# Performance work log

Measured on AMD Instinct MI355X. Metric: run time of the kernel, lower is better.

The kernel has to match this reference:

```python
import jax, jax.numpy as jnp
import numpy as np

DIM, HEADS, DH, P, C = 2048, 8, 256, 7, 128
NP = (56 // P) ** 2          # 64 patches
N = NP + 1 + NP              # 65 pos tokens concatenated with 64 patch tokens = 129
PATCH_FEAT = C * P * P       # 6272
LN_EPS = 1e-5


def patchify(x, p):
    # 'b c (h p1) (w p2) -> b (h w) (p1 p2 c)'
    b, c, H, W = x.shape
    h, w = H // p, W // p
    x = x.reshape(b, c, h, p, w, p).transpose(0, 2, 4, 3, 5, 1)
    return x.reshape(b, h * w, p * p * c)


def setup_inputs() -> dict:
    key = jax.random.key(0)
    ks = jax.random.split(key, 16)
    s = 0.02
    d = dict(
        x_q=jax.random.normal(ks[0], (64, C, 56, 56), jnp.float32),
        x_kv=jax.random.normal(ks[1], (64, C, 56, 56), jnp.float32),
        W_ex=jax.random.normal(ks[2], (PATCH_FEAT, DIM), jnp.float32) * s,
        b_ex=jnp.zeros((DIM,), jnp.float32),
        W_en=jax.random.normal(ks[3], (PATCH_FEAT, DIM), jnp.float32) * s,
        b_en=jnp.zeros((DIM,), jnp.float32),
        pos=jax.random.normal(ks[4], (1, NP + 1, DIM), jnp.float32),
        Wq=jax.random.normal(ks[5], (DIM, HEADS * DH), jnp.float32) * s,
        Wk=jax.random.normal(ks[6], (DIM, HEADS * DH), jnp.float32) * s,
        Wv=jax.random.normal(ks[7], (DIM, HEADS * DH), jnp.float32) * s,
        Wo=jax.random.normal(ks[8], (HEADS * DH, DIM), jnp.float32) * s,
        bo=jnp.zeros((DIM,), jnp.float32),
        gamma=jnp.ones((DIM,), jnp.float32),
        beta=jnp.zeros((DIM,), jnp.float32),
        Wh=jax.random.normal(ks[9], (DIM, PATCH_FEAT), jnp.float32) * s,
        bh=jnp.zeros((PATCH_FEAT,), jnp.float32),
        Wm=jax.random.normal(ks[10], (DH, N), jnp.float32) * s,
        bm=jnp.zeros((N,), jnp.float32),
    )
    return d


def reference(x_q, x_kv, W_ex, b_ex, W_en, b_en, pos, Wq, Wk, Wv, Wo, bo,
              gamma, beta, Wh, bh, Wm, bm):
    b = x_q.shape[0]
    scale = DH ** -0.5
    # image embedder: patch embed + concat pos tokens
    tq = patchify(x_q, P) @ W_ex + b_ex                      # [b, 64, DIM]
    tk = patchify(x_kv, P) @ W_en + b_en                     # [b, 64, DIM]
    posb = jnp.broadcast_to(pos, (b, NP + 1, DIM))
    tq = jnp.concatenate([posb, tq], axis=1)                 # [b, N, DIM]
    tk = jnp.concatenate([posb, tk], axis=1)                 # [b, N, DIM]

    def split_heads(t):
        return t.reshape(b, N, HEADS, DH).transpose(0, 2, 1, 3)  # b h n d

    q = split_heads(tq @ Wq)
    k = split_heads(tk @ Wk)
    v = split_heads(tk @ Wv)

    # VAE-style reparameterize: mu=k, logvar=q
    eps = jax.random.normal(jax.random.key(42), k.shape, k.dtype)
    z = k + jnp.exp(0.5 * q) * eps                           # [b, h, n, d]

    # scale + linear remap d -> N, softmax, weighted sum with v
    dots = (z * scale) @ Wm + bm                             # [b, h, n, N]
    attn = jax.nn.softmax(dots, axis=-1)
    out = jnp.einsum('bhij,bhjd->bhid', attn, v)             # [b, h, n, d]
    out = out.transpose(0, 2, 1, 3).reshape(b, N, HEADS * DH)
    out = out @ Wo + bo                                      # [b, N, DIM]

    # mlp head: LayerNorm + Linear (final rearrange-to-image is shape-only, omitted)
    mu = out.mean(-1, keepdims=True)
    var = ((out - mu) ** 2).mean(-1, keepdims=True)
    ln = (out - mu) * jax.lax.rsqrt(var + LN_EPS) * gamma + beta
    head = ln @ Wh + bh                                      # [b, N, 6272]

    qf = q.reshape(b, -1)
    kf = k.reshape(b, -1)
    qn = qf / jnp.linalg.norm(qf, axis=1, keepdims=True)
    kn = kf / jnp.linalg.norm(kf, axis=1, keepdims=True)
    return head, qn, kn
```

## Files before the change

kernel.cpp:

```cpp
#include <hip/hip_runtime.h>


typedef unsigned short u16;
typedef short bf16x8 __attribute__((ext_vector_type(8)));
typedef unsigned short u16x8 __attribute__((ext_vector_type(8)));
typedef float f32x4 __attribute__((ext_vector_type(4)));

#define WAITV(N) asm volatile("s_waitcnt vmcnt(" #N ")" ::: "memory")

static __device__ __forceinline__ void barx() {
    asm volatile("" ::: "memory");
    __builtin_amdgcn_s_barrier();
    asm volatile("" ::: "memory");
}

static __device__ __forceinline__ u16 f2b(float f) {
    union { float f; unsigned int u; } cv; cv.f = f;
    unsigned int u = cv.u;
    unsigned int lsb = (u >> 16) & 1u;
    u += 0x7fffu + lsb;
    return (u16)(u >> 16);
}

static __device__ __forceinline__ float b2f(u16 u) {
    union { unsigned int i; float f; } c; c.i = ((unsigned int)u) << 16; return c.f;
}

static __device__ __forceinline__ void gemm8p_body(
    const u16* __restrict__ A, const u16* __restrict__ Bt, void* __restrict__ Cv,
    const float* __restrict__ bias, int M, int N, int K,
    int lda, int ldb, int ldc, float alpha, int c_bf16, int row_remap,
    int m0, int n0, u16* lds)
{
    const int tid = threadIdx.x, lane = tid & 63, wave = tid >> 6;
    const int wm = wave >> 2, wn = wave & 3;
    const int l15 = lane & 15, l4 = lane >> 4;
    const int scol = (((lane & 3) ^ ((lane >> 3) & 3)) << 3);
    const int bswz = ((l4 ^ ((l15 >> 1) & 3)) << 3);

    f32x4 acc[8][4] = {};
    const int nt = K >> 6;
    const int niter = nt >> 1;

    auto STAGE = [&](int tt, int kh, int isB) {
        const int c = tt & 1;
        const int k0 = (tt << 6) + (kh << 5);
        const int rbase = isB ? n0 : m0;
        const u16* P = isB ? Bt : A;
        const int ld = isB ? ldb : lda;
        const int lim = isB ? N : M;
        const int dbase = c * 32768 + isB * 16384 + kh * 8192;
        #pragma unroll
        for (int j = 0; j < 2; ++j) {
            const int r0 = j * 128 + wave * 16;
            int g = rbase + r0 + (lane >> 2); g = g < lim ? g : lim - 1;
            const u16* src = P + (long)g * ld + k0 + scol;
            __builtin_amdgcn_global_load_lds(
                (const __attribute__((address_space(1))) void*)src,
                (__attribute__((address_space(3))) void*)&lds[dbase + r0 * 32],
                16, 0, 0);
        }
    };

    bf16x8 bfr[4];
    auto LOADB = [&](int c, int kk) {
        #pragma unroll
        for (int nn = 0; nn < 4; ++nn) {
            const int row = wn * 64 + nn * 16 + l15;
            bfr[nn] = *(const bf16x8*)&lds[c * 32768 + 16384 + kk * 8192 + row * 32 + bswz];
        }
    };
    auto LDA = [&](int c, int kk, int mh, bf16x8* af) {
        #pragma unroll
        for (int mm = 0; mm < 4; ++mm) {
            const int row = wm * 128 + mh * 64 + mm * 16 + l15;
            af[mm] = *(const bf16x8*)&lds[c * 32768 + kk * 8192 + row * 32 + bswz];
        }
    };
    auto MM = [&](const bf16x8* af, int mh) {
        __builtin_amdgcn_s_setprio(1);
        #pragma unroll
        for (int mm = 0; mm < 4; ++mm)
            #pragma unroll
            for (int nn = 0; nn < 4; ++nn)
                acc[mh * 4 + mm][nn] = __builtin_amdgcn_mfma_f32_16x16x32_bf16(
                    af[mm], bfr[nn], acc[mh * 4 + mm][nn], 0, 0, 0);
        __builtin_amdgcn_s_setprio(0);
    };

    STAGE(0, 0, 0); STAGE(0, 0, 1); STAGE(0, 1, 0); STAGE(0, 1, 1);
    STAGE(1, 0, 0); STAGE(1, 0, 1);

    bf16x8 a0[4], a1[4];
    for (int i = 0; i < niter; ++i) {
        const int t0 = 2 * i, t1 = t0 + 1;
        const bool has2 = (t0 + 2 < nt);
        WAITV(8); barx();
        LOADB(0, 0); LDA(0, 0, 0, a0);
        STAGE(t1, 1, 0); STAGE(t1, 1, 1);
        MM(a0, 0); LDA(0, 0, 1, a1); MM(a1, 1);
        WAITV(8); barx();
        LOADB(0, 1); LDA(0, 1, 0, a0);
        if (has2) { STAGE(t0 + 2, 0, 0); STAGE(t0 + 2, 0, 1); }
        MM(a0, 0); LDA(0, 1, 1, a1); MM(a1, 1);
        if (has2) { WAITV(8); } else { WAITV(4); }
        barx();
        LOADB(1, 0); LDA(1, 0, 0, a0);
        if (has2) { STAGE(t0 + 2, 1, 0); STAGE(t0 + 2, 1, 1); }
        MM(a0, 0); LDA(1, 0, 1, a1); MM(a1, 1);
        if (has2) { WAITV(8); } else { WAITV(0); }
        barx();
        LOADB(1, 1); LDA(1, 1, 0, a0);
        if (has2) { STAGE(t1 + 2, 0, 0); STAGE(t1 + 2, 0, 1); }
        MM(a0, 0); LDA(1, 1, 1, a1); MM(a1, 1);
    }

    #pragma unroll
    for (int mr = 0; mr < 8; ++mr) {
        #pragma unroll
        for (int nn = 0; nn < 4; ++nn) {
            const int col = n0 + wn * 64 + nn * 16 + l15;
            if (col >= N) continue;
            const float bv = bias ? bias[col] : 0.0f;
            #pragma unroll
            for (int jj = 0; jj < 4; ++jj) {
                const int row = m0 + wm * 128 + mr * 16 + l4 * 4 + jj;
                if (row >= M) continue;
                float v = alpha * acc[mr][nn][jj] + bv;
                long crow = row;
                if (row_remap) crow = (long)(row >> 6) * 129 + 65 + (row & 63);
                if (c_bf16) ((u16*)Cv)[crow * (long)ldc + col] = f2b(v);
                else        ((float*)Cv)[crow * (long)ldc + col] = v;
            }
        }
    }
}

__global__ __launch_bounds__(512, 2) void gemm_8p(
    const u16* __restrict__ A, const u16* __restrict__ Bt, void* __restrict__ Cv,
    const float* __restrict__ bias, int M, int N, int K,
    int lda, int ldb, int ldc, float alpha, int c_bf16, int row_remap)
{
    __shared__ u16 lds[65536];
    gemm8p_body(A, Bt, Cv, bias, M, N, K, lda, ldb, ldc, alpha, c_bf16, row_remap,
                blockIdx.x * 256, blockIdx.y * 256, lds);
}

__global__ __launch_bounds__(512, 2) void gemm_8p3(
    const u16* A0, const u16* A1, const u16* A2,
    const u16* B0, const u16* B1, const u16* B2,
    u16* C0, u16* C1, u16* C2,
    const float* bias0, const float* bias1, const float* bias2,
    int M, int N, int K, int lda, int ldb, int ldc, float alpha, int row_remap)
{
    __shared__ u16 lds[65536];
    const int z = blockIdx.z;
    const u16* A = z == 0 ? A0 : (z == 1 ? A1 : A2);
    const u16* B = z == 0 ? B0 : (z == 1 ? B1 : B2);
    u16* C = z == 0 ? C0 : (z == 1 ? C1 : C2);
    const float* bias = z == 0 ? bias0 : (z == 1 ? bias1 : bias2);
    gemm8p_body(A, B, C, bias, M, N, K, lda, ldb, ldc, alpha, 1, row_remap,
                blockIdx.x * 256, blockIdx.y * 256, lds);
}

__global__ __launch_bounds__(256, 2) void gemm_pipe(
    const u16* __restrict__ A, const u16* __restrict__ Bt, void* __restrict__ Cv,
    const float* __restrict__ bias, int M, int N, int K,
    int lda, int ldb, int ldc, float alpha, int c_bf16)
{
    __shared__ u16 lds[2 * 16384];

    const int tid = threadIdx.x, lane = tid & 63, wave = tid >> 6;
    const int wm = wave >> 1, wn = wave & 1;
    const int l15 = lane & 15, l4 = lane >> 4;

    const int srow = tid >> 3;
    const int scol = (((tid & 7) * 16) ^ (((tid >> 3) & 7) << 4)) >> 1;
    const int cf0 = (((0 * 64) + l4 * 16) ^ ((l15 & 7) << 4)) >> 1;
    const int cf1 = (((1 * 64) + l4 * 16) ^ ((l15 & 7) << 4)) >> 1;

    const int nt = K >> 6;
    const int nbx = (M + 127) >> 7, nby = N >> 7;
    const int ntiles = nbx * nby;

    for (int tile = blockIdx.x; tile < ntiles; tile += gridDim.x) {
        const int m0 = (tile / nby) * 128, n0 = (tile % nby) * 128;

        auto STAGE = [&](int c, int t) {
            const int k0 = t << 6;
            #pragma unroll
            for (int j = 0; j < 4; ++j) {
                const int r = j * 32 + srow;
                int ga = m0 + r; ga = ga < M ? ga : M - 1;
                const u16* srcA = A + (long)ga * lda + k0 + scol;
                __builtin_amdgcn_global_load_lds(
                    (const __attribute__((address_space(1))) void*)srcA,
                    (__attribute__((address_space(3))) void*)&lds[c * 16384 + j * 2048 + wave * 512],
                    16, 0, 0);
                int gb = n0 + r; gb = gb < N ? gb : N - 1;
                const u16* srcB = Bt + (long)gb * ldb + k0 + scol;
                __builtin_amdgcn_global_load_lds(
                    (const __attribute__((address_space(1))) void*)srcB,
                    (__attribute__((address_space(3))) void*)&lds[c * 16384 + 8192 + j * 2048 + wave * 512],
                    16, 0, 0);
            }
        };

        f32x4 acc[4][4] = {};
        STAGE(0, 0);
        __syncthreads();
        for (int t = 0; t < nt; ++t) {
            const int c = t & 1;
            if (t + 1 < nt) STAGE(c ^ 1, t + 1);
            const int ab = c * 16384, bb = ab + 8192;
            #pragma unroll
            for (int kk = 0; kk < 2; ++kk) {
                const int cf = kk ? cf1 : cf0;
                bf16x8 af[4], bfr[4];
                #pragma unroll
                for (int m = 0; m < 4; ++m)
                    af[m] = *(const bf16x8*)&lds[ab + (wm * 64 + m * 16 + l15) * 64 + cf];
                #pragma unroll
                for (int n = 0; n < 4; ++n)
                    bfr[n] = *(const bf16x8*)&lds[bb + (wn * 64 + n * 16 + l15) * 64 + cf];
                __builtin_amdgcn_s_setprio(1);
                #pragma unroll
                for (int m = 0; m < 4; ++m)
                    #pragma unroll
                    for (int n = 0; n < 4; ++n)
                        acc[m][n] = __builtin_amdgcn_mfma_f32_16x16x32_bf16(
                            af[m], bfr[n], acc[m][n], 0, 0, 0);
                __builtin_amdgcn_s_setprio(0);
            }
            __syncthreads();
        }

        #pragma unroll
        for (int m = 0; m < 4; ++m) {
            #pragma unroll
            for (int n = 0; n < 4; ++n) {
                const int col = n0 + wn * 64 + n * 16 + l15;
                if (col >= N) continue;
                const float bv = bias ? bias[col] : 0.0f;
                #pragma unroll
                for (int j = 0; j < 4; ++j) {
                    const int row = m0 + wm * 64 + m * 16 + l4 * 4 + j;
                    if (row >= M) continue;
                    float v = alpha * acc[m][n][j] + bv;
                    if (c_bf16) ((u16*)Cv)[(long)row * ldc + col] = f2b(v);
                    else        ((float*)Cv)[(long)row * ldc + col] = v;
                }
            }
        }
    }
}

__global__ __launch_bounds__(256) void gemm_bt(
    const u16* __restrict__ A, const u16* __restrict__ Bt, void* __restrict__ Cv,
    const float* __restrict__ bias, int M, int N, int K,
    int lda, int ldb, int ldc, float alpha, int c_bf16, int row_remap,
    long sA, long sB, long sCo, long sCi, int binner)
{
    const int bz = blockIdx.z;
    const u16* Ab = A + (long)bz * sA;
    const u16* Bb = Bt + (long)bz * sB;
    const long cOff = (long)(bz / binner) * sCo + (long)(bz % binner) * sCi;

    __shared__ u16 As[128][72];
    __shared__ u16 Bs[128][72];

    const int tid = threadIdx.x;
    const int lane = tid & 63;
    const int wave = tid >> 6;
    const int wr = wave >> 1, wc = wave & 1;
    const int l15 = lane & 15, l4 = lane >> 4;
    const int m0 = blockIdx.x * 128, n0 = blockIdx.y * 128;

    const int r = tid >> 3;
    const int kof = (tid & 7) * 8;

    f32x4 acc[4][4] = {};

    const int ktiles = (K + 63) / 64;
    for (int kt = 0; kt < ktiles; ++kt) {
        const int k0 = kt * 64;
        __syncthreads();
        #pragma unroll
        for (int i = 0; i < 4; ++i) {
            const int row = r + 32 * i;
            const int gk = k0 + kof;
            u16x8 v = {0,0,0,0,0,0,0,0};
            const int grow = m0 + row;
            if (grow < M && gk < K)
                v = *(const u16x8*)(Ab + (long)grow * lda + gk);
            *(u16x8*)&As[row][kof] = v;
        }
        #pragma unroll
        for (int i = 0; i < 4; ++i) {
            const int row = r + 32 * i;
            const int gk = k0 + kof;
            u16x8 v = {0,0,0,0,0,0,0,0};
            const int gcol = n0 + row;
            if (gcol < N && gk < K)
                v = *(const u16x8*)(Bb + (long)gcol * ldb + gk);
            *(u16x8*)&Bs[row][kof] = v;
        }
        __syncthreads();
        #pragma unroll
        for (int ks = 0; ks < 2; ++ks) {
            bf16x8 af[4], bfr[4];
            #pragma unroll
            for (int m = 0; m < 4; ++m)
                af[m] = *(const bf16x8*)&As[wr*64 + m*16 + l15][ks*32 + l4*8];
            #pragma unroll
            for (int n = 0; n < 4; ++n)
                bfr[n] = *(const bf16x8*)&Bs[wc*64 + n*16 + l15][ks*32 + l4*8];
            #pragma unroll
            for (int m = 0; m < 4; ++m)
                #pragma unroll
                for (int n = 0; n < 4; ++n)
                    acc[m][n] = __builtin_amdgcn_mfma_f32_16x16x32_bf16(
                        af[m], bfr[n], acc[m][n], 0, 0, 0);
        }
    }

    #pragma unroll
    for (int m = 0; m < 4; ++m) {
        #pragma unroll
        for (int n = 0; n < 4; ++n) {
            const int col = n0 + wc*64 + n*16 + l15;
            if (col >= N) continue;
            const float bv = bias ? bias[col] : 0.0f;
            #pragma unroll
            for (int j = 0; j < 4; ++j) {
                const int row = m0 + wr*64 + m*16 + l4*4 + j;
                if (row >= M) continue;
                float v = alpha * acc[m][n][j] + bv;
                long crow = row;
                if (row_remap) crow = (long)(row >> 6) * 129 + 65 + (row & 63);
                if (c_bf16) ((u16*)Cv)[cOff + crow * (long)ldc + col] = f2b(v);
                else        ((float*)Cv)[cOff + crow * (long)ldc + col] = v;
            }
        }
    }
}

__global__ __launch_bounds__(256, 2) void fdots_kernel(
    const u16* __restrict__ z, const u16* __restrict__ Wm_t,
    const float* __restrict__ bm, u16* __restrict__ attn)
{
    __shared__ u16 wlds[144 * 264];
    const int tid = threadIdx.x;
    for (int i = tid; i < 144 * 32; i += 256) {
        const int row = i >> 5, c8 = i & 31;
        *(u16x8*)&wlds[row * 264 + c8 * 8] = *(const u16x8*)&Wm_t[row * 256 + c8 * 8];
    }
    __syncthreads();
    const int lane = tid & 63, wave = tid >> 6;
    const int l15 = lane & 15, l4 = lane >> 4;

    float bmv[9];
    #pragma unroll
    for (int c = 0; c < 9; ++c) {
        const int col = c * 16 + l15;
        bmv[c] = (col < 129) ? bm[col] : 0.0f;
    }

    for (int rg = blockIdx.x; rg < 516; rg += gridDim.x) {
        const long rowbase = (long)rg * 128 + wave * 32;

        f32x4 acc[2][9] = {};
        #pragma unroll
        for (int kk = 0; kk < 8; ++kk) {
            bf16x8 af[2];
            #pragma unroll
            for (int rgp = 0; rgp < 2; ++rgp)
                af[rgp] = *(const bf16x8*)&z[(rowbase + rgp * 16 + l15) * 256 + kk * 32 + l4 * 8];
            #pragma unroll
            for (int c = 0; c < 9; ++c) {
                const bf16x8 bf = *(const bf16x8*)&wlds[(c * 16 + l15) * 264 + kk * 32 + l4 * 8];
                #pragma unroll
                for (int rgp = 0; rgp < 2; ++rgp)
                    acc[rgp][c] = __builtin_amdgcn_mfma_f32_16x16x32_bf16(af[rgp], bf, acc[rgp][c], 0, 0, 0);
            }
        }

        #pragma unroll
        for (int rgp = 0; rgp < 2; ++rgp) {
            #pragma unroll
            for (int j = 0; j < 4; ++j) {
                float v[9]; float mx = -1e30f;
                #pragma unroll
                for (int c = 0; c < 9; ++c) {
                    const int col = c * 16 + l15;
                    v[c] = (col < 129) ? (0.0625f * acc[rgp][c][j] + bmv[c]) : -1e30f;
                    mx = fmaxf(mx, v[c]);
                }
                #pragma unroll
                for (int o = 1; o < 16; o <<= 1) mx = fmaxf(mx, __shfl_xor(mx, o, 64));
                float s = 0.f;
                #pragma unroll
                for (int c = 0; c < 9; ++c) {
                    v[c] = (c * 16 + l15 < 129) ? expf(v[c] - mx) : 0.0f;
                    s += v[c];
                }
                #pragma unroll
                for (int o = 1; o < 16; o <<= 1) s += __shfl_xor(s, o, 64);
                const float inv = 1.0f / s;
                u16* ar = attn + (rowbase + rgp * 16 + l4 * 4 + j) * 144;
                #pragma unroll
                for (int c = 0; c < 9; ++c)
                    ar[c * 16 + l15] = f2b(v[c] * inv);
            }
        }
    }
}

__global__ __launch_bounds__(256) void row128_kernel(
    const u16* __restrict__ attn, const u16* __restrict__ v_t, u16* __restrict__ outm)
{
    const int bh = blockIdx.x, d = threadIdx.x;
    const int b = bh >> 3, h = bh & 7;
    __shared__ float a[144];
    for (int j = threadIdx.x; j < 144; j += 256)
        a[j] = (j < 129) ? b2f(attn[((long)bh * 129 + 128) * 144 + j]) : 0.0f;
    __syncthreads();
    const u16* vr = v_t + ((long)bh * 256 + d) * 144;
    float s = 0.f;
    #pragma unroll
    for (int j8 = 0; j8 < 18; ++j8) {
        const bf16x8 vv = *(const bf16x8*)&vr[j8 * 8];
        #pragma unroll
        for (int e = 0; e < 8; ++e) s += a[j8 * 8 + e] * b2f((u16)vv[e]);
    }
    outm[((long)(b * 129 + 128)) * 2048 + h * 256 + d] = f2b(s);
}

__global__ __launch_bounds__(256) void transpose_conv4(
    const float* in0, const float* in1, const float* in2, const float* in3,
    u16* o0, u16* o1, u16* o2, u16* o3, int K, int N, int KP, int NPd)
{
    const int zz = blockIdx.z;
    const float* in = zz == 0 ? in0 : (zz == 1 ? in1 : (zz == 2 ? in2 : in3));
    u16* out = zz == 0 ? o0 : (zz == 1 ? o1 : (zz == 2 ? o2 : o3));
    __shared__ float tile[32][33];
    const int k0 = blockIdx.x * 32, n0 = blockIdx.y * 32;
    const int tx = threadIdx.x, ty = threadIdx.y;
    #pragma unroll
    for (int i = 0; i < 4; ++i) {
        const int k = k0 + ty + i*8, n = n0 + tx;
        tile[ty + i*8][tx] = (k < K && n < N) ? in[(long)k * N + n] : 0.0f;
    }
    __syncthreads();
    #pragma unroll
    for (int i = 0; i < 4; ++i) {
        const int n = n0 + ty + i*8, k = k0 + tx;
        if (n < NPd && k < KP) out[(long)n * KP + k] = f2b(tile[tx][ty + i*8]);
    }
}

__global__ __launch_bounds__(256) void patchify_kernel(
    const float* __restrict__ xq, const float* __restrict__ xkv,
    u16* __restrict__ oq, u16* __restrict__ okv)
{
    __shared__ u16 tile[64 * 7 * 58];
    const int zz = blockIdx.z;
    const float* x = (zz >= 64) ? xkv : xq;
    u16* out = (zz >= 64) ? okv : oq;
    const int b = zz & 63, hh = blockIdx.y, cg = blockIdx.x;
    const int c0 = cg * 64;
    for (int i = threadIdx.x; i < 64 * 392; i += 256) {
        const int c = i / 392, rem = i - c * 392;
        const int p1 = rem / 56, w = rem - p1 * 56;
        const float v = x[(((long)b * 128 + c0 + c) * 56 + hh * 7 + p1) * 56 + w];
        tile[(c * 7 + p1) * 58 + w] = f2b(v);
    }
    __syncthreads();
    #pragma unroll
    for (int ww = 0; ww < 8; ++ww) {
        const long base = ((long)(b * 64 + hh * 8 + ww)) * 6272 + c0;
        for (int j = threadIdx.x; j < 49 * 64; j += 256) {
            const int c = j & 63, pp = j >> 6;
            const int p1 = pp / 7, p2 = pp - p1 * 7;
            out[base + pp * 128 + c] = tile[(c * 7 + p1) * 58 + ww * 7 + p2];
        }
    }
}

__global__ __launch_bounds__(256) void posfill_kernel(
    const float* __restrict__ pos, u16* __restrict__ Tq, u16* __restrict__ Tk)
{
    const int t = blockIdx.x, b = blockIdx.y;
    const int c0 = threadIdx.x * 8;
    const float* pr = pos + (long)t * 2048 + c0;
    u16x8 v;
    #pragma unroll
    for (int e = 0; e < 8; ++e) v[e] = f2b(pr[e]);
    const long idx = ((long)b * 129 + t) * 2048 + c0;
    *(u16x8*)&Tq[idx] = v;
    *(u16x8*)&Tk[idx] = v;
}

__global__ void vtrans_kernel(const u16* __restrict__ vmat, u16* __restrict__ v_t)
{
    const int bh = blockIdx.z; const int b = bh >> 3, h = bh & 7;
    const int d0 = blockIdx.x * 32, n0 = blockIdx.y * 32;
    __shared__ u16 tile[32][33];
    const int tx = threadIdx.x, ty = threadIdx.y;
    #pragma unroll
    for (int i = 0; i < 4; ++i) {
        const int n = n0 + ty + i*8;
        if (n < 129)
            tile[ty + i*8][tx] = vmat[((long)b*129 + n) * 2048 + h*256 + d0 + tx];
    }
    __syncthreads();
    #pragma unroll
    for (int i = 0; i < 4; ++i) {
        const int d = d0 + ty + i*8, n = n0 + tx;
        if (n < 144)
            v_t[((long)bh * 256 + d) * 144 + n] = (n < 129) ? tile[tx][ty + i*8] : (u16)0;
    }
}

static __device__ __forceinline__ unsigned int rotl32(unsigned int x, int d) {
    return (x << d) | (x >> (32 - d));
}

static __device__ __forceinline__ float threefry_normal(unsigned int i) {
    const unsigned int ks0 = 0u, ks1 = 42u;
    const unsigned int ks2 = ks0 ^ ks1 ^ 0x1BD11BDAu;
    unsigned int x0 = 0u + ks0;
    unsigned int x1 = i + ks1;
#define TF_R(rr) { x0 += x1; x1 = rotl32(x1, rr); x1 ^= x0; }
    TF_R(13) TF_R(15) TF_R(26) TF_R(6)
    x0 += ks1; x1 += ks2 + 1u;
    TF_R(17) TF_R(29) TF_R(16) TF_R(24)
    x0 += ks2; x1 += ks0 + 2u;
    TF_R(13) TF_R(15) TF_R(26) TF_R(6)
    x0 += ks0; x1 += ks1 + 3u;
    TF_R(17) TF_R(29) TF_R(16) TF_R(24)
    x0 += ks1; x1 += ks2 + 4u;
    TF_R(13) TF_R(15) TF_R(26) TF_R(6)
    x0 += ks2; x1 += ks0 + 5u;
#undef TF_R
    const unsigned int bits = x0 ^ x1;
    const unsigned int fb = (bits >> 9) | 0x3f800000u;
    union { unsigned int u; float f; } cv; cv.u = fb;
    const float f = cv.f - 1.0f;
    const float lo = -0.99999994f;
    float u = f * (1.0f - lo) + lo;
    u = fmaxf(lo, u);
    return 1.4142135623730951f * erfinvf(u);
}

__global__ __launch_bounds__(256) void z_kernel(
    const u16* __restrict__ qmat, const u16* __restrict__ kmat,
    const float* __restrict__ norms, u16* __restrict__ z,
    float* __restrict__ outq, float* __restrict__ outk)
{
    const unsigned int i = blockIdx.x * 256u + threadIdx.x;
    const int d = i & 255; const unsigned int t = i >> 8;
    const int n = t % 129; const int bh = t / 129;
    const int b = bh >> 3, h = bh & 7;
    const long src = ((long)(b * 129 + n)) * 2048 + h * 256 + d;
    const float qf = b2f(qmat[src]);
    const float kf = b2f(kmat[src]);
    const float eps = threefry_normal(i);
    z[i] = f2b(kf + expf(0.5f * qf) * eps);
    outq[i] = qf / norms[b];
    outk[i] = kf / norms[64 + b];
}

__global__ __launch_bounds__(256) void ln_kernel(
    const float* __restrict__ proj, const float* __restrict__ gamma,
    const float* __restrict__ beta, u16* __restrict__ ln)
{
    const int row = blockIdx.x;
    const float* p = proj + (long)row * 2048;
    const int tid = threadIdx.x;
    float v[8]; float s = 0.f, s2 = 0.f;
    #pragma unroll
    for (int i = 0; i < 8; ++i) {
        v[i] = p[tid + i * 256]; s += v[i]; s2 += v[i] * v[i];
    }
    #pragma unroll
    for (int o = 32; o > 0; o >>= 1) { s += __shfl_down(s, o, 64); s2 += __shfl_down(s2, o, 64); }
    __shared__ float sh[8];
    if ((tid & 63) == 0) { sh[tid >> 6] = s; sh[4 + (tid >> 6)] = s2; }
    __syncthreads();
    s = sh[0] + sh[1] + sh[2] + sh[3];
    s2 = sh[4] + sh[5] + sh[6] + sh[7];
    const float mu = s * (1.0f / 2048.0f);
    const float var = s2 * (1.0f / 2048.0f) - mu * mu;
    const float rinv = 1.0f / sqrtf(var + 1e-5f);
    u16* lr = ln + (long)row * 2048;
    #pragma unroll
    for (int i = 0; i < 8; ++i) {
        const int c = tid + i * 256;
        lr[c] = f2b((v[i] - mu) * rinv * gamma[c] + beta[c]);
    }
}

__global__ __launch_bounds__(256) void norm_reduce(
    const u16* __restrict__ qmat, const u16* __restrict__ kmat, float* __restrict__ norms)
{
    const int b = blockIdx.x & 63;
    const u16* src = (blockIdx.x >= 64 ? kmat : qmat) + (long)b * 264192;
    float s = 0.f;
    for (int i = threadIdx.x; i < 264192; i += 256) { const float x = b2f(src[i]); s += x * x; }
    #pragma unroll
    for (int o = 32; o > 0; o >>= 1) s += __shfl_down(s, o, 64);
    __shared__ float sh[4];
    if ((threadIdx.x & 63) == 0) sh[threadIdx.x >> 6] = s;
    __syncthreads();
    if (threadIdx.x == 0) norms[blockIdx.x] = sqrtf(sh[0] + sh[1] + sh[2] + sh[3]);
}

extern "C" void kernel_launch(void* const* d_in, const int* in_sizes, int n_in,
                              void* d_out, int out_size, void* d_ws, size_t ws_size,
                              hipStream_t stream)
{
    const float* x_q   = (const float*)d_in[0];
    const float* x_kv  = (const float*)d_in[1];
    const float* W_ex  = (const float*)d_in[2];
    const float* b_ex  = (const float*)d_in[3];
    const float* W_en  = (const float*)d_in[4];
    const float* b_en  = (const float*)d_in[5];
    const float* pos   = (const float*)d_in[6];
    const float* Wq    = (const float*)d_in[7];
    const float* Wk    = (const float*)d_in[8];
    const float* Wv    = (const float*)d_in[9];
    const float* Wo    = (const float*)d_in[10];
    const float* bo    = (const float*)d_in[11];
    const float* gamma = (const float*)d_in[12];
    const float* beta  = (const float*)d_in[13];
    const float* Wh    = (const float*)d_in[14];
    const float* bh    = (const float*)d_in[15];
    const float* Wm    = (const float*)d_in[16];
    const float* bm    = (const float*)d_in[17];
    (void)in_sizes; (void)n_in; (void)out_size; (void)ws_size;

    char* ws = (char*)d_ws;
    size_t off = 0;
    auto alloc = [&](size_t bytes) -> char* {
        char* p = ws + off;
        off += (bytes + 255) & ~(size_t)255;
        return p;
    };
    u16*   Xq_p  = (u16*)alloc(4096UL * 6272 * 2);
    u16*   Xk_p  = (u16*)alloc(4096UL * 6272 * 2);
    u16*   Wex_t = (u16*)alloc(2048UL * 6272 * 2);
    u16*   Wen_t = (u16*)alloc(2048UL * 6272 * 2);
    u16*   Tq    = (u16*)alloc(8256UL * 2048 * 2);
    u16*   Tk    = (u16*)alloc(8256UL * 2048 * 2);
    u16*   Wq_t  = (u16*)alloc(2048UL * 2048 * 2);
    u16*   Wk_t  = (u16*)alloc(2048UL * 2048 * 2);
    u16*   Wv_t  = (u16*)alloc(2048UL * 2048 * 2);
    u16*   qmat  = (u16*)alloc(8256UL * 2048 * 2);
    u16*   kmat  = (u16*)alloc(8256UL * 2048 * 2);
    u16*   vmat  = (u16*)alloc(8256UL * 2048 * 2);
    u16*   v_t   = (u16*)alloc(512UL * 256 * 144 * 2);
    u16*   z     = (u16*)alloc(66048UL * 256 * 2);
    u16*   attn  = (u16*)alloc(66048UL * 144 * 2);
    u16*   outm  = (u16*)alloc(8256UL * 2048 * 2);
    float* proj  = (float*)alloc(8256UL * 2048 * 4);
    u16*   ln    = (u16*)alloc(8256UL * 2048 * 2);
    u16*   Wo_t  = (u16*)alloc(2048UL * 2048 * 2);
    u16*   Wh_t  = (u16*)alloc(6272UL * 2048 * 2);
    u16*   Wm_t  = (u16*)alloc(144UL * 256 * 2);
    float* norms = (float*)alloc(128UL * 4);

    transpose_conv4<<<dim3(196, 64, 2), dim3(32, 8), 0, stream>>>(
        W_ex, W_en, W_ex, W_en, Wex_t, Wen_t, Wex_t, Wen_t, 6272, 2048, 6272, 2048);
    patchify_kernel<<<dim3(2, 8, 128), 256, 0, stream>>>(x_q, x_kv, Xq_p, Xk_p);
    posfill_kernel<<<dim3(65, 64), 256, 0, stream>>>(pos, Tq, Tk);

    gemm_8p3<<<dim3(16, 8, 2), 512, 0, stream>>>(
        Xq_p, Xk_p, Xk_p, Wex_t, Wen_t, Wen_t, Tq, Tk, Tk,
        b_ex, b_en, b_en, 4096, 2048, 6272, 6272, 6272, 2048, 1.0f, 1);

    transpose_conv4<<<dim3(64, 64, 4), dim3(32, 8), 0, stream>>>(
        Wq, Wk, Wv, Wo, Wq_t, Wk_t, Wv_t, Wo_t, 2048, 2048, 2048, 2048);
    gemm_8p3<<<dim3(33, 8, 3), 512, 0, stream>>>(
        Tq, Tk, Tk, Wq_t, Wk_t, Wv_t, qmat, kmat, vmat,
        nullptr, nullptr, nullptr, 8256, 2048, 2048, 2048, 2048, 2048, 1.0f, 0);

    vtrans_kernel<<<dim3(8, 5, 512), dim3(32, 8), 0, stream>>>(vmat, v_t);

    norm_reduce<<<128, 256, 0, stream>>>(qmat, kmat, norms);
    {
        float* outq = (float*)d_out + 51781632L;
        float* outk = outq + 16908288L;
        z_kernel<<<66048, 256, 0, stream>>>(qmat, kmat, norms, z, outq, outk);
    }

    transpose_conv4<<<dim3(8, 5, 1), dim3(32, 8), 0, stream>>>(
        Wm, Wm, Wm, Wm, Wm_t, Wm_t, Wm_t, Wm_t, 256, 129, 256, 144);
    fdots_kernel<<<512, 256, 0, stream>>>(z, Wm_t, bm, attn);

    {
        dim3 grid(1, 2, 512);
        gemm_bt<<<grid, 256, 0, stream>>>(attn, v_t, outm, nullptr,
            128, 256, 144, 144, 144, 2048, 1.0f, 1, 0,
            129L * 144, 256L * 144, 129L * 2048, 256L, 8);
    }
    row128_kernel<<<512, 256, 0, stream>>>(attn, v_t, outm);

    gemm_pipe<<<1024, 256, 0, stream>>>(
        outm, Wo_t, proj, bo, 8256, 2048, 2048, 2048, 2048, 2048, 1.0f, 0);

    ln_kernel<<<8256, 256, 0, stream>>>(proj, gamma, beta, ln);

    transpose_conv4<<<dim3(64, 196, 1), dim3(32, 8), 0, stream>>>(
        Wh, Wh, Wh, Wh, Wh_t, Wh_t, Wh_t, Wh_t, 2048, 6272, 2048, 6272);
    gemm_8p<<<dim3(33, 25), 512, 0, stream>>>(
        ln, Wh_t, (float*)d_out, bh, 8256, 6272, 2048, 2048, 2048, 6272, 1.0f, 0, 0);
}
```

Baseline: 1.598 ms.

## Replace pipelined 256x256 GEMMs with simple single-buffered 128x128 GEMM kernel

All large GEMMs (embedding, QKV, output projection, head) now go through one single-buffered 128x128-tile kernel with 4 waves and a sync-load-sync-compute loop. This replaces the 8-wave 256x256 double-buffered pipeline and the persistent double-buffered gemm_pipe. The change removes the load/compute overlap and cuts per-tile data reuse, in exchange for simpler code, more blocks and smaller LDS. It reads as a simplification or a baseline comparison, and it risks exposing global memory latency in every K step.

```diff
diff --git a/kernel.cpp b/kernel.cpp
--- a/kernel.cpp
+++ b/kernel.cpp
@@ -5,14 +5,6 @@
 typedef short bf16x8 __attribute__((ext_vector_type(8)));
 typedef unsigned short u16x8 __attribute__((ext_vector_type(8)));
 typedef float f32x4 __attribute__((ext_vector_type(4)));
-
-#define WAITV(N) asm volatile("s_waitcnt vmcnt(" #N ")" ::: "memory")
-
-static __device__ __forceinline__ void barx() {
-    asm volatile("" ::: "memory");
-    __builtin_amdgcn_s_barrier();
-    asm volatile("" ::: "memory");
-}
 
 static __device__ __forceinline__ u16 f2b(float f) {
     union { float f; unsigned int u; } cv; cv.f = f;
@@ -26,107 +18,77 @@
     union { unsigned int i; float f; } c; c.i = ((unsigned int)u) << 16; return c.f;
 }
 
-static __device__ __forceinline__ void gemm8p_body(
+static __device__ __forceinline__ void gemm_sb_body(
     const u16* __restrict__ A, const u16* __restrict__ Bt, void* __restrict__ Cv,
     const float* __restrict__ bias, int M, int N, int K,
     int lda, int ldb, int ldc, float alpha, int c_bf16, int row_remap,
     int m0, int n0, u16* lds)
 {
     const int tid = threadIdx.x, lane = tid & 63, wave = tid >> 6;
-    const int wm = wave >> 2, wn = wave & 3;
+    const int wm = wave >> 1, wn = wave & 1;
     const int l15 = lane & 15, l4 = lane >> 4;
-    const int scol = (((lane & 3) ^ ((lane >> 3) & 3)) << 3);
-    const int bswz = ((l4 ^ ((l15 >> 1) & 3)) << 3);
-
-    f32x4 acc[8][4] = {};
+
+    const int srow = tid >> 3;
+    const int scol = (((tid & 7) * 16) ^ ((srow & 7) << 4)) >> 1;
+    const int cf0 = (((0 * 64) + l4 * 16) ^ ((l15 & 7) << 4)) >> 1;
+    const int cf1 = (((1 * 64) + l4 * 16) ^ ((l15 & 7) << 4)) >> 1;
+
+    f32x4 acc[4][4] = {};
     const int nt = K >> 6;
-    const int niter = nt >> 1;
-
-    auto STAGE = [&](int tt, int kh, int isB) {
-        const int c = tt & 1;
-        const int k0 = (tt << 6) + (kh << 5);
-        const int rbase = isB ? n0 : m0;
-        const u16* P = isB ? Bt : A;
-        const int ld = isB ? ldb : lda;
-        const int lim = isB ? N : M;
-        const int dbase = c * 32768 + isB * 16384 + kh * 8192;
-        #pragma unroll
-        for (int j = 0; j < 2; ++j) {
-            const int r0 = j * 128 + wave * 16;
-            int g = rbase + r0 + (lane >> 2); g = g < lim ? g : lim - 1;
-            const u16* src = P + (long)g * ld + k0 + scol;
+
+    for (int t = 0; t < nt; ++t) {
+        const int k0 = t << 6;
+        __syncthreads();
+        #pragma unroll
+        for (int j = 0; j < 4; ++j) {
+            const int r = j * 32 + srow;
+            int ga = m0 + r; ga = ga < M ? ga : M - 1;
+            const u16* srcA = A + (long)ga * lda + k0 + scol;
             __builtin_amdgcn_global_load_lds(
-                (const __attribute__((address_space(1))) void*)src,
-                (__attribute__((address_space(3))) void*)&lds[dbase + r0 * 32],
+                (const __attribute__((address_space(1))) void*)srcA,
+                (__attribute__((address_space(3))) void*)&lds[j * 2048 + wave * 512],
                 16, 0, 0);
-        }
-    };
-
-    bf16x8 bfr[4];
-    auto LOADB = [&](int c, int kk) {
-        #pragma unroll
-        for (int nn = 0; nn < 4; ++nn) {
-            const int row = wn * 64 + nn * 16 + l15;
-            bfr[nn] = *(const bf16x8*)&lds[c * 32768 + 16384 + kk * 8192 + row * 32 + bswz];
-        }
-    };
-    auto LDA = [&](int c, int kk, int mh, bf16x8* af) {
-        #pragma unroll
-        for (int mm = 0; mm < 4; ++mm) {
-            const int row = wm * 128 + mh * 64 + mm * 16 + l15;
-            af[mm] = *(const bf16x8*)&lds[c * 32768 + kk * 8192 + row * 32 + bswz];
-        }
-    };
-    auto MM = [&](const bf16x8* af, int mh) {
-        __builtin_amdgcn_s_setprio(1);
-        #pragma unroll
-        for (int mm = 0; mm < 4; ++mm)
-            #pragma unroll
-            for (int nn = 0; nn < 4; ++nn)
-                acc[mh * 4 + mm][nn] = __builtin_amdgcn_mfma_f32_16x16x32_bf16(
-                    af[mm], bfr[nn], acc[mh * 4 + mm][nn], 0, 0, 0);
-        __builtin_amdgcn_s_setprio(0);
-    };
-
-    STAGE(0, 0, 0); STAGE(0, 0, 1); STAGE(0, 1, 0); STAGE(0, 1, 1);
-    STAGE(1, 0, 0); STAGE(1, 0, 1);
-
-    bf16x8 a0[4], a1[4];
-    for (int i = 0; i < niter; ++i) {
-        const int t0 = 2 * i, t1 = t0 + 1;
-        const bool has2 = (t0 + 2 < nt);
-        WAITV(8); barx();
-        LOADB(0, 0); LDA(0, 0, 0, a0);
-        STAGE(t1, 1, 0); STAGE(t1, 1, 1);
-        MM(a0, 0); LDA(0, 0, 1, a1); MM(a1, 1);
-        WAITV(8); barx();
-        LOADB(0, 1); LDA(0, 1, 0, a0);
-        if (has2) { STAGE(t0 + 2, 0, 0); STAGE(t0 + 2, 0, 1); }
-        MM(a0, 0); LDA(0, 1, 1, a1); MM(a1, 1);
-        if (has2) { WAITV(8); } else { WAITV(4); }
-        barx();
-        LOADB(1, 0); LDA(1, 0, 0, a0);
-        if (has2) { STAGE(t0 + 2, 1, 0); STAGE(t0 + 2, 1, 1); }
-        MM(a0, 0); LDA(1, 0, 1, a1); MM(a1, 1);
-        if (has2) { WAITV(8); } else { WAITV(0); }
-        barx();
-        LOADB(1, 1); LDA(1, 1, 0, a0);
-        if (has2) { STAGE(t1 + 2, 0, 0); STAGE(t1 + 2, 0, 1); }
-        MM(a0, 0); LDA(1, 1, 1, a1); MM(a1, 1);
-    }
-
-    #pragma unroll
-    for (int mr = 0; mr < 8; ++mr) {
-        #pragma unroll
-        for (int nn = 0; nn < 4; ++nn) {
-            const int col = n0 + wn * 64 + nn * 16 + l15;
+            int gb = n0 + r; gb = gb < N ? gb : N - 1;
+            const u16* srcB = Bt + (long)gb * ldb + k0 + scol;
+            __builtin_amdgcn_global_load_lds(
+                (const __attribute__((address_space(1))) void*)srcB,
+                (__attribute__((address_space(3))) void*)&lds[8192 + j * 2048 + wave * 512],
+                16, 0, 0);
+        }
+        __syncthreads();
+        #pragma unroll
+        for (int kk = 0; kk < 2; ++kk) {
+            const int cf = kk ? cf1 : cf0;
+            bf16x8 af[4], bfr[4];
+            #pragma unroll
+            for (int m = 0; m < 4; ++m)
+                af[m] = *(const bf16x8*)&lds[(wm * 64 + m * 16 + l15) * 64 + cf];
+            #pragma unroll
+            for (int n = 0; n < 4; ++n)
+                bfr[n] = *(const bf16x8*)&lds[8192 + (wn * 64 + n * 16 + l15) * 64 + cf];
+            __builtin_amdgcn_s_setprio(1);
+            #pragma unroll
+            for (int m = 0; m < 4; ++m)
+                #pragma unroll
+                for (int n = 0; n < 4; ++n)
+                    acc[m][n] = __builtin_amdgcn_mfma_f32_16x16x32_bf16(
+                        af[m], bfr[n], acc[m][n], 0, 0, 0);
+            __builtin_amdgcn_s_setprio(0);
+        }
+    }
+
+    #pragma unroll
+    for (int m = 0; m < 4; ++m) {
+        #pragma unroll
+        for (int n = 0; n < 4; ++n) {
+            const int col = n0 + wn * 64 + n * 16 + l15;
             if (col >= N) continue;
             const float bv = bias ? bias[col] : 0.0f;
             #pragma unroll
-            for (int jj = 0; jj < 4; ++jj) {
-                const int row = m0 + wm * 128 + mr * 16 + l4 * 4 + jj;
+            for (int j = 0; j < 4; ++j) {
+                const int row = m0 + wm * 64 + m * 16 + l4 * 4 + j;
                 if (row >= M) continue;
-                float v = alpha * acc[mr][nn][jj] + bv;
+                float v = alpha * acc[m][n][j] + bv;
                 long crow = row;
                 if (row_remap) crow = (long)(row >> 6) * 129 + 65 + (row & 63);
                 if (c_bf16) ((u16*)Cv)[crow * (long)ldc + col] = f2b(v);
@@ -136,123 +98,31 @@
     }
 }
 
-__global__ __launch_bounds__(512, 2) void gemm_8p(
+__global__ __launch_bounds__(256) void gemm_sb(
     const u16* __restrict__ A, const u16* __restrict__ Bt, void* __restrict__ Cv,
     const float* __restrict__ bias, int M, int N, int K,
     int lda, int ldb, int ldc, float alpha, int c_bf16, int row_remap)
 {
-    __shared__ u16 lds[65536];
-    gemm8p_body(A, Bt, Cv, bias, M, N, K, lda, ldb, ldc, alpha, c_bf16, row_remap,
-                blockIdx.x * 256, blockIdx.y * 256, lds);
-}
-
-__global__ __launch_bounds__(512, 2) void gemm_8p3(
+    __shared__ u16 lds[16384];
+    gemm_sb_body(A, Bt, Cv, bias, M, N, K, lda, ldb, ldc, alpha, c_bf16,
+                 row_remap, blockIdx.x * 128, blockIdx.y * 128, lds);
+}
+
+__global__ __launch_bounds__(256) void gemm_sb3(
     const u16* A0, const u16* A1, const u16* A2,
     const u16* B0, const u16* B1, const u16* B2,
     u16* C0, u16* C1, u16* C2,
     const float* bias0, const float* bias1, const float* bias2,
     int M, int N, int K, int lda, int ldb, int ldc, float alpha, int row_remap)
 {
-    __shared__ u16 lds[65536];
+    __shared__ u16 lds[16384];
     const int z = blockIdx.z;
     const u16* A = z == 0 ? A0 : (z == 1 ? A1 : A2);
     const u16* B = z == 0 ? B0 : (z == 1 ? B1 : B2);
     u16* C = z == 0 ? C0 : (z == 1 ? C1 : C2);
     const float* bias = z == 0 ? bias0 : (z == 1 ? bias1 : bias2);
-    gemm8p_body(A, B, C, bias, M, N, K, lda, ldb, ldc, alpha, 1, row_remap,
-                blockIdx.x * 256, blockIdx.y * 256, lds);
-}
-
-__global__ __launch_bounds__(256, 2) void gemm_pipe(
-    const u16* __restrict__ A, const u16* __restrict__ Bt, void* __restrict__ Cv,
-    const float* __restrict__ bias, int M, int N, int K,
-    int lda, int ldb, int ldc, float alpha, int c_bf16)
-{
-    __shared__ u16 lds[2 * 16384];
-
-    const int tid = threadIdx.x, lane = tid & 63, wave = tid >> 6;
-    const int wm = wave >> 1, wn = wave & 1;
-    const int l15 = lane & 15, l4 = lane >> 4;
-
-    const int srow = tid >> 3;
-    const int scol = (((tid & 7) * 16) ^ (((tid >> 3) & 7) << 4)) >> 1;
-    const int cf0 = (((0 * 64) + l4 * 16) ^ ((l15 & 7) << 4)) >> 1;
-    const int cf1 = (((1 * 64) + l4 * 16) ^ ((l15 & 7) << 4)) >> 1;
-
-    const int nt = K >> 6;
-    const int nbx = (M + 127) >> 7, nby = N >> 7;
-    const int ntiles = nbx * nby;
-
-    for (int tile = blockIdx.x; tile < ntiles; tile += gridDim.x) {
-        const int m0 = (tile / nby) * 128, n0 = (tile % nby) * 128;
-
-        auto STAGE = [&](int c, int t) {
-            const int k0 = t << 6;
-            #pragma unroll
-            for (int j = 0; j < 4; ++j) {
-                const int r = j * 32 + srow;
-                int ga = m0 + r; ga = ga < M ? ga : M - 1;
-                const u16* srcA = A + (long)ga * lda + k0 + scol;
-                __builtin_amdgcn_global_load_lds(
-                    (const __attribute__((address_space(1))) void*)srcA,
-                    (__attribute__((address_space(3))) void*)&lds[c * 16384 + j * 2048 + wave * 512],
-                    16, 0, 0);
-                int gb = n0 + r; gb = gb < N ? gb : N - 1;
-                const u16* srcB = Bt + (long)gb * ldb + k0 + scol;
-                __builtin_amdgcn_global_load_lds(
-                    (const __attribute__((address_space(1))) void*)srcB,
-                    (__attribute__((address_space(3))) void*)&lds[c * 16384 + 8192 + j * 2048 + wave * 512],
-                    16, 0, 0);
-            }
-        };
-
-        f32x4 acc[4][4] = {};
-        STAGE(0, 0);
-        __syncthreads();
-        for (int t = 0; t < nt; ++t) {
-            const int c = t & 1;
-            if (t + 1 < nt) STAGE(c ^ 1, t + 1);
-            const int ab = c * 16384, bb = ab + 8192;
-            #pragma unroll
-            for (int kk = 0; kk < 2; ++kk) {
-                const int cf = kk ? cf1 : cf0;
-                bf16x8 af[4], bfr[4];
-                #pragma unroll
-                for (int m = 0; m < 4; ++m)
-                    af[m] = *(const bf16x8*)&lds[ab + (wm * 64 + m * 16 + l15) * 64 + cf];
-                #pragma unroll
-                for (int n = 0; n < 4; ++n)
-                    bfr[n] = *(const bf16x8*)&lds[bb + (wn * 64 + n * 16 + l15) * 64 + cf];
-                __builtin_amdgcn_s_setprio(1);
-                #pragma unroll
-                for (int m = 0; m < 4; ++m)
-                    #pragma unroll
-                    for (int n = 0; n < 4; ++n)
-                        acc[m][n] = __builtin_amdgcn_mfma_f32_16x16x32_bf16(
-                            af[m], bfr[n], acc[m][n], 0, 0, 0);
-                __builtin_amdgcn_s_setprio(0);
-            }
-            __syncthreads();
-        }
-
-        #pragma unroll
-        for (int m = 0; m < 4; ++m) {
-            #pragma unroll
-            for (int n = 0; n < 4; ++n) {
-                const int col = n0 + wn * 64 + n * 16 + l15;
-                if (col >= N) continue;
-                const float bv = bias ? bias[col] : 0.0f;
-                #pragma unroll
-                for (int j = 0; j < 4; ++j) {
-                    const int row = m0 + wm * 64 + m * 16 + l4 * 4 + j;
-                    if (row >= M) continue;
-                    float v = alpha * acc[m][n][j] + bv;
-                    if (c_bf16) ((u16*)Cv)[(long)row * ldc + col] = f2b(v);
-                    else        ((float*)Cv)[(long)row * ldc + col] = v;
-                }
-            }
-        }
-    }
+    gemm_sb_body(A, B, C, bias, M, N, K, lda, ldb, ldc, alpha, 1, row_remap,
+                 blockIdx.x * 128, blockIdx.y * 128, lds);
 }
 
 __global__ __launch_bounds__(256) void gemm_bt(
@@ -675,13 +545,13 @@
     patchify_kernel<<<dim3(2, 8, 128), 256, 0, stream>>>(x_q, x_kv, Xq_p, Xk_p);
     posfill_kernel<<<dim3(65, 64), 256, 0, stream>>>(pos, Tq, Tk);
 
-    gemm_8p3<<<dim3(16, 8, 2), 512, 0, stream>>>(
+    gemm_sb3<<<dim3(32, 16, 2), 256, 0, stream>>>(
         Xq_p, Xk_p, Xk_p, Wex_t, Wen_t, Wen_t, Tq, Tk, Tk,
         b_ex, b_en, b_en, 4096, 2048, 6272, 6272, 6272, 2048, 1.0f, 1);
 
     transpose_conv4<<<dim3(64, 64, 4), dim3(32, 8), 0, stream>>>(
         Wq, Wk, Wv, Wo, Wq_t, Wk_t, Wv_t, Wo_t, 2048, 2048, 2048, 2048);
-    gemm_8p3<<<dim3(33, 8, 3), 512, 0, stream>>>(
+    gemm_sb3<<<dim3(65, 16, 3), 256, 0, stream>>>(
         Tq, Tk, Tk, Wq_t, Wk_t, Wv_t, qmat, kmat, vmat,
         nullptr, nullptr, nullptr, 8256, 2048, 2048, 2048, 2048, 2048, 1.0f, 0);
 
@@ -706,13 +576,13 @@
     }
     row128_kernel<<<512, 256, 0, stream>>>(attn, v_t, outm);
 
-    gemm_pipe<<<1024, 256, 0, stream>>>(
-        outm, Wo_t, proj, bo, 8256, 2048, 2048, 2048, 2048, 2048, 1.0f, 0);
+    gemm_sb<<<dim3(65, 16), 256, 0, stream>>>(
+        outm, Wo_t, proj, bo, 8256, 2048, 2048, 2048, 2048, 2048, 1.0f, 0, 0);
 
     ln_kernel<<<8256, 256, 0, stream>>>(proj, gamma, beta, ln);
 
     transpose_conv4<<<dim3(64, 196, 1), dim3(32, 8), 0, stream>>>(
         Wh, Wh, Wh, Wh, Wh_t, Wh_t, Wh_t, Wh_t, 2048, 6272, 2048, 6272);
-    gemm_8p<<<dim3(33, 25), 512, 0, stream>>>(
+    gemm_sb<<<dim3(65, 49), 256, 0, stream>>>(
         ln, Wh_t, (float*)d_out, bh, 8256, 6272, 2048, 2048, 2048, 6272, 1.0f, 0, 0);
 }
```

After: 1.765 ms. +10.5%, slower.
